# Performance work log

Hardware: AMD Instinct MI355X
Metric: run time of the kernel (lower is better)

The kernel has to match this reference:

```python
import jax, jax.numpy as jnp
import numpy as np


def setup_inputs() -> dict:
    key = jax.random.key(0)
    k1, k2 = jax.random.split(key)
    B, C, H, W = 1, 3, 3500, 2500
    src = jax.random.normal(k1, (B, C, H, W), dtype=jnp.float32)
    flow = jax.random.normal(k2, (B, 2, H, W), dtype=jnp.float32)
    return {"src": src, "flow": flow}


def reference(src, flow):
    """SpatialTransformer.forward: flow + identity grid -> normalize -> bilinear
    grid_sample (zeros padding, align_corners=True). Returns (warped, norm_grid).
    src:  [B, C, H, W] float
    flow: [B, 2, H, W] float; channel 0 = x (width) displacement, channel 1 = y.
    """
    B, C, H, W = src.shape
    dt = flow.dtype
    xs = jnp.arange(W, dtype=dt)  # identity x coords
    ys = jnp.arange(H, dtype=dt)  # identity y coords
    gx = flow[:, 0] + xs[None, None, :]  # [B, H, W] absolute x coord
    gy = flow[:, 1] + ys[None, :, None]  # [B, H, W] absolute y coord
    # normalize to [-1, 1]; max_extent = (W-1, H-1) per torch code
    nx = 2.0 * gx / (W - 1) - 1.0
    ny = 2.0 * gy / (H - 1) - 1.0
    norm_grid = jnp.stack([nx, ny], axis=-1)  # [B, H, W, 2], second output

    # grid_sample with align_corners=True: unnormalize back to pixel coords
    ix = (nx + 1.0) * 0.5 * (W - 1)
    iy = (ny + 1.0) * 0.5 * (H - 1)
    x0 = jnp.floor(ix)
    y0 = jnp.floor(iy)
    x1 = x0 + 1.0
    y1 = y0 + 1.0
    wx1 = ix - x0
    wx0 = 1.0 - wx1
    wy1 = iy - y0
    wy0 = 1.0 - wy1

    def gather(xi, yi):
        # zeros padding: out-of-range corners contribute 0
        valid = (xi >= 0) & (xi <= W - 1) & (yi >= 0) & (yi <= H - 1)
        xc = jnp.clip(xi, 0, W - 1).astype(jnp.int32)
        yc = jnp.clip(yi, 0, H - 1).astype(jnp.int32)
        vals = jax.vmap(lambda sb, yb, xb: sb[:, yb, xb])(src, yc, xc)  # [B,C,H,W]
        return vals * valid.astype(src.dtype)[:, None]

    out = (gather(x0, y0) * (wx0 * wy0)[:, None]
           + gather(x1, y0) * (wx1 * wy0)[:, None]
           + gather(x0, y1) * (wx0 * wy1)[:, None]
           + gather(x1, y1) * (wx1 * wy1)[:, None])
    return out, norm_grid
```

## Files before the change

### kernel.cpp

```cpp
#include <hip/hip_runtime.h>

#define HH 3500
#define WW 2500
#define TXs 64
#define TYs 16
#define WIN_H 24
#define WIN_W 76
#define WIN_W4 (WIN_W/4)
#define NSTG (3*WIN_H*WIN_W4)
#define NTX ((WW + TXs - 1)/TXs)
#define NTY ((HH + TYs - 1)/TYs)
#define NXCD 8

typedef float f32x4 __attribute__((ext_vector_type(4)));

__global__ __launch_bounds__(256, 7) void st_warp_v10(
    const float* __restrict__ src,
    const float* __restrict__ flow,
    float* __restrict__ out)
{
    __shared__ float sm[3][WIN_H][WIN_W];

    const int nwg = NTX * NTY;
    const int cpx = nwg / NXCD;
    const int bid = blockIdx.x;
    const int sbid = (bid % NXCD) * cpx + bid / NXCD;
    const int xt = sbid / NTY;
    const int yt = sbid - xt * NTY;

    const int tx0 = xt * TXs;
    const int ty0 = yt * TYs;
    const int cx0 = tx0 - 4;
    const int ry0 = ty0 - 4;

    const int wxlo = max(cx0, 0);
    const int wxhi = min(cx0 + WIN_W - 1, WW - 1);
    const int wylo = max(ry0, 0);
    const int wyhi = min(ry0 + WIN_H - 1, HH - 1);

    const long HW = (long)HH * WW;
    const int tid = threadIdx.x;
    const bool colsafe = (cx0 >= 0) && (cx0 + WIN_W <= WW);

    const int r  = tid >> 4;
    const int xb = tx0 + (tid & 15) * 4;
    const int y  = ty0 + r;
    const bool active = (xb < WW) && (y < HH);
    const long idx = (long)y * WW + xb;

    f32x4 fx4 = {0,0,0,0}, fy4 = {0,0,0,0};
    if (active) {
        fx4 = *reinterpret_cast<const f32x4*>(flow + idx);
        fy4 = *reinterpret_cast<const f32x4*>(flow + HW + idx);
    }

    if (colsafe) {
#pragma unroll
        for (int i = 0; i < 6; ++i) {
            const int e = tid + i * 256;
            if (e < NSTG) {
                const int c   = e / (WIN_H * WIN_W4);
                const int rem = e - c * (WIN_H * WIN_W4);
                const int rr  = rem / WIN_W4;
                const int v   = rem - rr * WIN_W4;
                int gy = ry0 + rr; gy = min(max(gy, 0), HH - 1);
                const f32x4 val = *reinterpret_cast<const f32x4*>(
                    src + (long)c * HW + (long)gy * WW + (cx0 + 4 * v));
                *reinterpret_cast<f32x4*>(&sm[c][rr][4 * v]) = val;
            }
        }
    } else {
        for (int e = tid; e < 3 * WIN_H * WIN_W; e += 256) {
            const int c   = e / (WIN_H * WIN_W);
            const int rem = e - c * (WIN_H * WIN_W);
            const int rr  = rem / WIN_W;
            const int j   = rem - rr * WIN_W;
            int gy = ry0 + rr; gy = min(max(gy, 0), HH - 1);
            int gx = cx0 + j;  gx = min(max(gx, 0), WW - 1);
            sm[c][rr][j] = src[(long)c * HW + (long)gy * WW + gx];
        }
    }

    float w00[4], w10[4], w01[4], w11[4];
    float ngv[8];
    int   lb[4];
    int   p0[4];
    int   p1[4];
    int   inwin_mask = 0;

    if (active) {
#pragma unroll
        for (int k = 0; k < 4; ++k) {
            const int x = xb + k;
            const float gx = fx4[k] + (float)x;
            const float gy = fy4[k] + (float)y;

            const float nx = 2.0f * gx / (float)(WW - 1) - 1.0f;
            const float ny = 2.0f * gy / (float)(HH - 1) - 1.0f;
            ngv[2 * k]     = nx;
            ngv[2 * k + 1] = ny;

            const float ixp = (nx + 1.0f) * 0.5f * (float)(WW - 1);
            const float iyp = (ny + 1.0f) * 0.5f * (float)(HH - 1);

            const float x0f = floorf(ixp), y0f = floorf(iyp);
            const float wx1 = ixp - x0f, wx0 = 1.0f - wx1;
            const float wy1 = iyp - y0f, wy0 = 1.0f - wy1;

            const int x0 = (int)x0f, y0i = (int)y0f;
            const int x1 = x0 + 1,  y1i = y0i + 1;

            const bool vx0 = (x0  >= 0) & (x0  < WW);
            const bool vx1 = (x1  >= 0) & (x1  < WW);
            const bool vy0 = (y0i >= 0) & (y0i < HH);
            const bool vy1 = (y1i >= 0) & (y1i < HH);

            w00[k] = wx0 * wy0 * ((vx0 & vy0) ? 1.0f : 0.0f);
            w10[k] = wx1 * wy0 * ((vx1 & vy0) ? 1.0f : 0.0f);
            w01[k] = wx0 * wy1 * ((vx0 & vy1) ? 1.0f : 0.0f);
            w11[k] = wx1 * wy1 * ((vx1 & vy1) ? 1.0f : 0.0f);

            const int x0c = min(max(x0,  0), WW - 1);
            const int y0c = min(max(y0i, 0), HH - 1);
            const int x1c = min(max(x1,  0), WW - 1);
            const int y1c = min(max(y1i, 0), HH - 1);
            p0[k] = (y0c << 16) | x0c;
            p1[k] = (y1c << 16) | x1c;

            const bool inwin = (x0 >= wxlo) & (x1 <= wxhi) &
                               (y0i >= wylo) & (y1i <= wyhi);
            inwin_mask |= (inwin ? 1 : 0) << k;

            lb[k] = (y0i - ry0) * WIN_W + (x0 - cx0);
        }
    }

    __syncthreads();

    if (!active) return;

#pragma unroll
    for (int c = 0; c < 3; ++c) {
        const float* __restrict__ buf = &sm[c][0][0];
        float o[4];
#pragma unroll
        for (int k = 0; k < 4; ++k) {
            if ((inwin_mask >> k) & 1) {
                const float* b = buf + lb[k];
                o[k] = b[0] * w00[k] + b[1] * w10[k]
                     + b[WIN_W] * w01[k] + b[WIN_W + 1] * w11[k];
            } else {
                const int x0c = p0[k] & 0xffff, y0c = p0[k] >> 16;
                const int x1c = p1[k] & 0xffff, y1c = p1[k] >> 16;
                const float* __restrict__ s = src + (long)c * HW;
                o[k] = s[(long)y0c * WW + x0c] * w00[k]
                     + s[(long)y0c * WW + x1c] * w10[k]
                     + s[(long)y1c * WW + x0c] * w01[k]
                     + s[(long)y1c * WW + x1c] * w11[k];
            }
        }
        f32x4 v = {o[0], o[1], o[2], o[3]};
        __builtin_nontemporal_store(v, reinterpret_cast<f32x4*>(out + (long)c * HW + idx));
    }
    float* ngbase = out + 3 * HW + 2 * idx;
    f32x4 n0 = {ngv[0], ngv[1], ngv[2], ngv[3]};
    f32x4 n1 = {ngv[4], ngv[5], ngv[6], ngv[7]};
    __builtin_nontemporal_store(n0, reinterpret_cast<f32x4*>(ngbase));
    __builtin_nontemporal_store(n1, reinterpret_cast<f32x4*>(ngbase + 4));
}

extern "C" void kernel_launch(void* const* d_in, const int* in_sizes, int n_in,
                              void* d_out, int out_size, void* d_ws, size_t ws_size,
                              hipStream_t stream) {
    const float* src  = (const float*)d_in[0];
    const float* flow = (const float*)d_in[1];
    float* out = (float*)d_out;
    (void)d_ws; (void)ws_size; (void)in_sizes; (void)n_in; (void)out_size;

    dim3 block(256, 1, 1);
    dim3 grid(NTX * NTY, 1, 1);
    st_warp_v10<<<grid, block, 0, stream>>>(src, flow, out);
}
```

Before: 99.81 us.

## Process three row tiles per block with double-buffered LDS prefetch

Each workgroup now handles three vertically stacked 64x16 tiles instead of one. While the current tile is computed, the next tile's source window is prefetched into registers and its flow is loaded, then written to a second LDS buffer. This hides global load latency behind compute. The cost is double the LDS footprint, more registers, and the occupancy hint drops from 7 to 3 waves, which may reduce latency hiding from other blocks.

After: 112.4 us. 1.13x slower.

```diff
diff --git a/kernel.cpp b/kernel.cpp
--- a/kernel.cpp
+++ b/kernel.cpp
@@ -4,91 +4,100 @@
 #define WW 2500
 #define TXs 64
 #define TYs 16
+#define KT 3
 #define WIN_H 24
 #define WIN_W 76
-#define WIN_W4 (WIN_W/4)
-#define NSTG (3*WIN_H*WIN_W4)
-#define NTX ((WW + TXs - 1)/TXs)
-#define NTY ((HH + TYs - 1)/TYs)
+#define WIN_W4 19
+#define PLANE (WIN_H*WIN_W4)
+#define NSTG (3*PLANE)
+#define NTX 40
+#define NTYG 73
 #define NXCD 8
 
 typedef float f32x4 __attribute__((ext_vector_type(4)));
 
-__global__ __launch_bounds__(256, 7) void st_warp_v10(
+__global__ __launch_bounds__(256, 3) void st_warp_v11(
     const float* __restrict__ src,
     const float* __restrict__ flow,
     float* __restrict__ out)
 {
-    __shared__ float sm[3][WIN_H][WIN_W];
-
-    const int nwg = NTX * NTY;
+    __shared__ float sm[2][3][WIN_H][WIN_W];
+
+    const int nwg = NTX * NTYG;
     const int cpx = nwg / NXCD;
     const int bid = blockIdx.x;
     const int sbid = (bid % NXCD) * cpx + bid / NXCD;
-    const int xt = sbid / NTY;
-    const int yt = sbid - xt * NTY;
-
-    const int tx0 = xt * TXs;
-    const int ty0 = yt * TYs;
-    const int cx0 = tx0 - 4;
-    const int ry0 = ty0 - 4;
-
+    const int xt = sbid / NTYG;
+    const int yg = sbid - xt * NTYG;
+
+    const int tx0  = xt * TXs;
+    const int ty00 = yg * (KT * TYs);
+    const int cx0  = tx0 - 4;
     const int wxlo = max(cx0, 0);
     const int wxhi = min(cx0 + WIN_W - 1, WW - 1);
-    const int wylo = max(ry0, 0);
-    const int wyhi = min(ry0 + WIN_H - 1, HH - 1);
 
     const long HW = (long)HH * WW;
     const int tid = threadIdx.x;
     const bool colsafe = (cx0 >= 0) && (cx0 + WIN_W <= WW);
 
+    int sc[6], srr[6], sv4[6];
+#pragma unroll
+    for (int i = 0; i < 6; ++i) {
+        const int e = tid + i * 256;
+        const int c = e / PLANE;
+        const int rem = e - c * PLANE;
+        const int rr = rem / WIN_W4;
+        sc[i] = c; srr[i] = rr; sv4[i] = (rem - rr * WIN_W4) * 4;
+    }
+
     const int r  = tid >> 4;
     const int xb = tx0 + (tid & 15) * 4;
-    const int y  = ty0 + r;
-    const bool active = (xb < WW) && (y < HH);
-    const long idx = (long)y * WW + xb;
-
-    f32x4 fx4 = {0,0,0,0}, fy4 = {0,0,0,0};
-    if (active) {
-        fx4 = *reinterpret_cast<const f32x4*>(flow + idx);
-        fy4 = *reinterpret_cast<const f32x4*>(flow + HW + idx);
-    }
-
-    if (colsafe) {
+
+    auto stage_load = [&](int ty0, f32x4* pre) {
+        const int ry0 = ty0 - 4;
 #pragma unroll
         for (int i = 0; i < 6; ++i) {
-            const int e = tid + i * 256;
-            if (e < NSTG) {
-                const int c   = e / (WIN_H * WIN_W4);
-                const int rem = e - c * (WIN_H * WIN_W4);
-                const int rr  = rem / WIN_W4;
-                const int v   = rem - rr * WIN_W4;
-                int gy = ry0 + rr; gy = min(max(gy, 0), HH - 1);
-                const f32x4 val = *reinterpret_cast<const f32x4*>(
-                    src + (long)c * HW + (long)gy * WW + (cx0 + 4 * v));
-                *reinterpret_cast<f32x4*>(&sm[c][rr][4 * v]) = val;
-            }
-        }
-    } else {
+            if (tid + i * 256 < NSTG) {
+                int gy = ry0 + srr[i]; gy = min(max(gy, 0), HH - 1);
+                pre[i] = *reinterpret_cast<const f32x4*>(
+                    src + (long)sc[i] * HW + (long)gy * WW + (cx0 + sv4[i]));
+            }
+        }
+    };
+    auto stage_write = [&](int b, const f32x4* pre) {
+#pragma unroll
+        for (int i = 0; i < 6; ++i) {
+            if (tid + i * 256 < NSTG) {
+                *reinterpret_cast<f32x4*>(&sm[b][sc[i]][srr[i]][sv4[i]]) = pre[i];
+            }
+        }
+    };
+    auto stage_direct = [&](int b, int ty0) {
+        const int ry0 = ty0 - 4;
         for (int e = tid; e < 3 * WIN_H * WIN_W; e += 256) {
-            const int c   = e / (WIN_H * WIN_W);
+            const int c = e / (WIN_H * WIN_W);
             const int rem = e - c * (WIN_H * WIN_W);
-            const int rr  = rem / WIN_W;
-            const int j   = rem - rr * WIN_W;
+            const int rr = rem / WIN_W;
+            const int j = rem - rr * WIN_W;
             int gy = ry0 + rr; gy = min(max(gy, 0), HH - 1);
             int gx = cx0 + j;  gx = min(max(gx, 0), WW - 1);
-            sm[c][rr][j] = src[(long)c * HW + (long)gy * WW + gx];
-        }
-    }
-
-    float w00[4], w10[4], w01[4], w11[4];
-    float ngv[8];
-    int   lb[4];
-    int   p0[4];
-    int   p1[4];
-    int   inwin_mask = 0;
-
-    if (active) {
+            sm[b][c][rr][j] = src[(long)c * HW + (long)gy * WW + gx];
+        }
+    };
+
+    auto compute = [&](int ty0, int b, f32x4 fx4, f32x4 fy4) {
+        const int y = ty0 + r;
+        if (xb >= WW || y >= HH) return;
+        const int ry0 = ty0 - 4;
+        const int wylo = max(ry0, 0);
+        const int wyhi = min(ry0 + WIN_H - 1, HH - 1);
+        const long idx = (long)y * WW + xb;
+
+        float w00[4], w10[4], w01[4], w11[4];
+        float ngv[8];
+        int   lb[4], p0[4], p1[4];
+        int   inwin_mask = 0;
+
 #pragma unroll
         for (int k = 0; k < 4; ++k) {
             const int x = xb + k;
@@ -133,40 +142,76 @@
 
             lb[k] = (y0i - ry0) * WIN_W + (x0 - cx0);
         }
+
+#pragma unroll
+        for (int c = 0; c < 3; ++c) {
+            const float* __restrict__ buf = &sm[b][c][0][0];
+            float o[4];
+#pragma unroll
+            for (int k = 0; k < 4; ++k) {
+                if ((inwin_mask >> k) & 1) {
+                    const float* bp = buf + lb[k];
+                    o[k] = bp[0] * w00[k] + bp[1] * w10[k]
+                         + bp[WIN_W] * w01[k] + bp[WIN_W + 1] * w11[k];
+                } else {
+                    const int x0c = p0[k] & 0xffff, y0c = p0[k] >> 16;
+                    const int x1c = p1[k] & 0xffff, y1c = p1[k] >> 16;
+                    const float* __restrict__ s = src + (long)c * HW;
+                    o[k] = s[(long)y0c * WW + x0c] * w00[k]
+                         + s[(long)y0c * WW + x1c] * w10[k]
+                         + s[(long)y1c * WW + x0c] * w01[k]
+                         + s[(long)y1c * WW + x1c] * w11[k];
+                }
+            }
+            f32x4 v = {o[0], o[1], o[2], o[3]};
+            __builtin_nontemporal_store(v, reinterpret_cast<f32x4*>(out + (long)c * HW + idx));
+        }
+        float* ngbase = out + 3 * HW + 2 * idx;
+        f32x4 n0 = {ngv[0], ngv[1], ngv[2], ngv[3]};
+        f32x4 n1 = {ngv[4], ngv[5], ngv[6], ngv[7]};
+        __builtin_nontemporal_store(n0, reinterpret_cast<f32x4*>(ngbase));
+        __builtin_nontemporal_store(n1, reinterpret_cast<f32x4*>(ngbase + 4));
+    };
+
+    f32x4 fcx = {0,0,0,0}, fcy = {0,0,0,0};
+    {
+        const int y0t = ty00 + r;
+        if (xb < WW && y0t < HH) {
+            const long id0 = (long)y0t * WW + xb;
+            fcx = *reinterpret_cast<const f32x4*>(flow + id0);
+            fcy = *reinterpret_cast<const f32x4*>(flow + HW + id0);
+        }
+        if (colsafe) { f32x4 pre[6]; stage_load(ty00, pre); stage_write(0, pre); }
+        else         { stage_direct(0, ty00); }
     }
-
     __syncthreads();
 
-    if (!active) return;
-
-#pragma unroll
-    for (int c = 0; c < 3; ++c) {
-        const float* __restrict__ buf = &sm[c][0][0];
-        float o[4];
-#pragma unroll
-        for (int k = 0; k < 4; ++k) {
-            if ((inwin_mask >> k) & 1) {
-                const float* b = buf + lb[k];
-                o[k] = b[0] * w00[k] + b[1] * w10[k]
-                     + b[WIN_W] * w01[k] + b[WIN_W + 1] * w11[k];
-            } else {
-                const int x0c = p0[k] & 0xffff, y0c = p0[k] >> 16;
-                const int x1c = p1[k] & 0xffff, y1c = p1[k] >> 16;
-                const float* __restrict__ s = src + (long)c * HW;
-                o[k] = s[(long)y0c * WW + x0c] * w00[k]
-                     + s[(long)y0c * WW + x1c] * w10[k]
-                     + s[(long)y1c * WW + x0c] * w01[k]
-                     + s[(long)y1c * WW + x1c] * w11[k];
-            }
-        }
-        f32x4 v = {o[0], o[1], o[2], o[3]};
-        __builtin_nontemporal_store(v, reinterpret_cast<f32x4*>(out + (long)c * HW + idx));
+#pragma unroll
+    for (int t = 0; t < KT; ++t) {
+        const int b = t & 1;
+        f32x4 pre[6];
+        f32x4 fnx = {0,0,0,0}, fny = {0,0,0,0};
+
+        if (t < KT - 1) {
+            const int tyn = ty00 + (t + 1) * TYs;
+            if (colsafe) stage_load(tyn, pre);
+            else         stage_direct(b ^ 1, tyn);
+            const int yn = tyn + r;
+            if (xb < WW && yn < HH) {
+                const long idn = (long)yn * WW + xb;
+                fnx = *reinterpret_cast<const f32x4*>(flow + idn);
+                fny = *reinterpret_cast<const f32x4*>(flow + HW + idn);
+            }
+        }
+
+        compute(ty00 + t * TYs, b, fcx, fcy);
+
+        if (t < KT - 1) {
+            if (colsafe) stage_write(b ^ 1, pre);
+            fcx = fnx; fcy = fny;
+            __syncthreads();
+        }
     }
-    float* ngbase = out + 3 * HW + 2 * idx;
-    f32x4 n0 = {ngv[0], ngv[1], ngv[2], ngv[3]};
-    f32x4 n1 = {ngv[4], ngv[5], ngv[6], ngv[7]};
-    __builtin_nontemporal_store(n0, reinterpret_cast<f32x4*>(ngbase));
-    __builtin_nontemporal_store(n1, reinterpret_cast<f32x4*>(ngbase + 4));
 }
 
 extern "C" void kernel_launch(void* const* d_in, const int* in_sizes, int n_in,
@@ -178,6 +223,6 @@
     (void)d_ws; (void)ws_size; (void)in_sizes; (void)n_in; (void)out_size;
 
     dim3 block(256, 1, 1);
-    dim3 grid(NTX * NTY, 1, 1);
-    st_warp_v10<<<grid, block, 0, stream>>>(src, flow, out);
+    dim3 grid(NTX * NTYG, 1, 1);
+    st_warp_v11<<<grid, block, 0, stream>>>(src, flow, out);
 }
```

## Interleave channels in swizzled shared tile and read corners as float4

Applied to the files above, without the earlier changes.

Changes the shared-memory window from three separate channel planes to one interleaved layout: each pixel holds its three channel values padded to a float4, and an XOR swizzle on the column index spreads accesses across LDS banks. The bilinear gather then reads one float4 per corner instead of three scalar reads per corner, which cuts the number of LDS instructions. Flow loads become nontemporal, and the launch-bounds occupancy hint drops from 7 to 5 because the tile is larger (a fourth padding slot per pixel). The w11 validity expression gains a redundant `|| true` clause that does not change its value.

New measurement: 106.2 us. +6.4%, slower.

```diff
diff --git a/kernel.cpp b/kernel.cpp
--- a/kernel.cpp
+++ b/kernel.cpp
@@ -6,20 +6,25 @@
 #define TYs 16
 #define WIN_H 24
 #define WIN_W 76
-#define WIN_W4 (WIN_W/4)
-#define NSTG (3*WIN_H*WIN_W4)
-#define NTX ((WW + TXs - 1)/TXs)
-#define NTY ((HH + TYs - 1)/TYs)
+#define WIN_W4 19
+#define ROWW (WIN_W*4)
+#define NUNIT (WIN_H*WIN_W4)
+#define NTX 40
+#define NTY 219
 #define NXCD 8
 
 typedef float f32x4 __attribute__((ext_vector_type(4)));
 
-__global__ __launch_bounds__(256, 7) void st_warp_v10(
+__device__ __forceinline__ int swz(int q) {
+    return (q << 2) ^ (q & 8) ^ ((q & 16) >> 2);
+}
+
+__global__ __launch_bounds__(256, 5) void st_warp_v12(
     const float* __restrict__ src,
     const float* __restrict__ flow,
     float* __restrict__ out)
 {
-    __shared__ float sm[3][WIN_H][WIN_W];
+    __shared__ float smw[WIN_H * ROWW];
 
     const int nwg = NTX * NTY;
     const int cpx = nwg / NXCD;
@@ -50,42 +55,49 @@
 
     f32x4 fx4 = {0,0,0,0}, fy4 = {0,0,0,0};
     if (active) {
-        fx4 = *reinterpret_cast<const f32x4*>(flow + idx);
-        fy4 = *reinterpret_cast<const f32x4*>(flow + HW + idx);
+        fx4 = __builtin_nontemporal_load(reinterpret_cast<const f32x4*>(flow + idx));
+        fy4 = __builtin_nontemporal_load(reinterpret_cast<const f32x4*>(flow + HW + idx));
     }
 
     if (colsafe) {
 #pragma unroll
-        for (int i = 0; i < 6; ++i) {
-            const int e = tid + i * 256;
-            if (e < NSTG) {
-                const int c   = e / (WIN_H * WIN_W4);
-                const int rem = e - c * (WIN_H * WIN_W4);
-                const int rr  = rem / WIN_W4;
-                const int v   = rem - rr * WIN_W4;
+        for (int i = 0; i < 2; ++i) {
+            const int u = tid + i * 256;
+            if (u < NUNIT) {
+                const int rr = u / WIN_W4;
+                const int v  = u - rr * WIN_W4;
                 int gy = ry0 + rr; gy = min(max(gy, 0), HH - 1);
-                const f32x4 val = *reinterpret_cast<const f32x4*>(
-                    src + (long)c * HW + (long)gy * WW + (cx0 + 4 * v));
-                *reinterpret_cast<f32x4*>(&sm[c][rr][4 * v]) = val;
+                const float* base = src + (long)gy * WW + (cx0 + 4 * v);
+                const f32x4 a = *reinterpret_cast<const f32x4*>(base);
+                const f32x4 b = *reinterpret_cast<const f32x4*>(base + HW);
+                const f32x4 c = *reinterpret_cast<const f32x4*>(base + 2 * HW);
+                const int q0 = 4 * v;
+                const int wbase = rr * ROWW;
+#pragma unroll
+                for (int j = 0; j < 4; ++j) {
+                    f32x4 t = {a[j], b[j], c[j], 0.0f};
+                    *reinterpret_cast<f32x4*>(&smw[wbase + swz(q0 + j)]) = t;
+                }
             }
         }
     } else {
-        for (int e = tid; e < 3 * WIN_H * WIN_W; e += 256) {
-            const int c   = e / (WIN_H * WIN_W);
-            const int rem = e - c * (WIN_H * WIN_W);
-            const int rr  = rem / WIN_W;
-            const int j   = rem - rr * WIN_W;
+        for (int e = tid; e < WIN_H * WIN_W; e += 256) {
+            const int rr = e / WIN_W;
+            const int q  = e - rr * WIN_W;
             int gy = ry0 + rr; gy = min(max(gy, 0), HH - 1);
-            int gx = cx0 + j;  gx = min(max(gx, 0), WW - 1);
-            sm[c][rr][j] = src[(long)c * HW + (long)gy * WW + gx];
+            int gx = cx0 + q;  gx = min(max(gx, 0), WW - 1);
+            const int w = rr * ROWW + swz(q);
+#pragma unroll
+            for (int c = 0; c < 3; ++c)
+                smw[w + c] = src[(long)c * HW + (long)gy * WW + gx];
         }
     }
 
     float w00[4], w10[4], w01[4], w11[4];
     float ngv[8];
-    int   lb[4];
-    int   p0[4];
-    int   p1[4];
+    int   lw[4];
+    int   lw1[4];
+    int   p0[4], p1[4];
     int   inwin_mask = 0;
 
     if (active) {
@@ -118,7 +130,7 @@
             w00[k] = wx0 * wy0 * ((vx0 & vy0) ? 1.0f : 0.0f);
             w10[k] = wx1 * wy0 * ((vx1 & vy0) ? 1.0f : 0.0f);
             w01[k] = wx0 * wy1 * ((vx0 & vy1) ? 1.0f : 0.0f);
-            w11[k] = wx1 * wy1 * ((vx1 & vy1) ? 1.0f : 0.0f);
+            w11[k] = wx1 * wy1 * ((vx0 || true ? (vx1 & vy1) : false) ? 1.0f : 0.0f);
 
             const int x0c = min(max(x0,  0), WW - 1);
             const int y0c = min(max(y0i, 0), HH - 1);
@@ -131,7 +143,10 @@
                                (y0i >= wylo) & (y1i <= wyhi);
             inwin_mask |= (inwin ? 1 : 0) << k;
 
-            lb[k] = (y0i - ry0) * WIN_W + (x0 - cx0);
+            const int rr = y0i - ry0;
+            const int q0 = x0 - cx0;
+            lw[k]  = rr * ROWW + swz(q0);
+            lw1[k] = rr * ROWW + swz(q0 + 1);
         }
     }
 
@@ -139,29 +154,37 @@
 
     if (!active) return;
 
-#pragma unroll
-    for (int c = 0; c < 3; ++c) {
-        const float* __restrict__ buf = &sm[c][0][0];
-        float o[4];
-#pragma unroll
-        for (int k = 0; k < 4; ++k) {
-            if ((inwin_mask >> k) & 1) {
-                const float* b = buf + lb[k];
-                o[k] = b[0] * w00[k] + b[1] * w10[k]
-                     + b[WIN_W] * w01[k] + b[WIN_W + 1] * w11[k];
-            } else {
-                const int x0c = p0[k] & 0xffff, y0c = p0[k] >> 16;
-                const int x1c = p1[k] & 0xffff, y1c = p1[k] >> 16;
+    float o0[4], o1[4], o2[4];
+#pragma unroll
+    for (int k = 0; k < 4; ++k) {
+        f32x4 ov;
+        if ((inwin_mask >> k) & 1) {
+            const f32x4 c00 = *reinterpret_cast<const f32x4*>(&smw[lw[k]]);
+            const f32x4 c10 = *reinterpret_cast<const f32x4*>(&smw[lw1[k]]);
+            const f32x4 c01 = *reinterpret_cast<const f32x4*>(&smw[lw[k]  + ROWW]);
+            const f32x4 c11 = *reinterpret_cast<const f32x4*>(&smw[lw1[k] + ROWW]);
+            ov = c00 * w00[k] + c10 * w10[k] + c01 * w01[k] + c11 * w11[k];
+        } else {
+            const int x0c = p0[k] & 0xffff, y0c = p0[k] >> 16;
+            const int x1c = p1[k] & 0xffff, y1c = p1[k] >> 16;
+            const long o00 = (long)y0c * WW + x0c, o10 = (long)y0c * WW + x1c;
+            const long o01 = (long)y1c * WW + x0c, o11 = (long)y1c * WW + x1c;
+#pragma unroll
+            for (int c = 0; c < 3; ++c) {
                 const float* __restrict__ s = src + (long)c * HW;
-                o[k] = s[(long)y0c * WW + x0c] * w00[k]
-                     + s[(long)y0c * WW + x1c] * w10[k]
-                     + s[(long)y1c * WW + x0c] * w01[k]
-                     + s[(long)y1c * WW + x1c] * w11[k];
+                ov[c] = s[o00] * w00[k] + s[o10] * w10[k]
+                      + s[o01] * w01[k] + s[o11] * w11[k];
             }
         }
-        f32x4 v = {o[0], o[1], o[2], o[3]};
-        __builtin_nontemporal_store(v, reinterpret_cast<f32x4*>(out + (long)c * HW + idx));
-    }
+        o0[k] = ov[0]; o1[k] = ov[1]; o2[k] = ov[2];
+    }
+
+    f32x4 v0 = {o0[0], o0[1], o0[2], o0[3]};
+    f32x4 v1 = {o1[0], o1[1], o1[2], o1[3]};
+    f32x4 v2 = {o2[0], o2[1], o2[2], o2[3]};
+    __builtin_nontemporal_store(v0, reinterpret_cast<f32x4*>(out + idx));
+    __builtin_nontemporal_store(v1, reinterpret_cast<f32x4*>(out + HW + idx));
+    __builtin_nontemporal_store(v2, reinterpret_cast<f32x4*>(out + 2 * HW + idx));
     float* ngbase = out + 3 * HW + 2 * idx;
     f32x4 n0 = {ngv[0], ngv[1], ngv[2], ngv[3]};
     f32x4 n1 = {ngv[4], ngv[5], ngv[6], ngv[7]};
@@ -179,5 +202,5 @@
 
     dim3 block(256, 1, 1);
     dim3 grid(NTX * NTY, 1, 1);
-    st_warp_v10<<<grid, block, 0, stream>>>(src, flow, out);
+    st_warp_v12<<<grid, block, 0, stream>>>(src, flow, out);
 }
```
